# Kernel optimization log

Measured on AMD Instinct MI355X. Metric: run time of the kernel, lower is better.

The kernel has to match this reference:

```python
import jax, jax.numpy as jnp
import numpy as np


def _maxpool2(x):
    # 2x2 max pool, stride 2, on NCHW
    b, c, h, w = x.shape
    return x.reshape(b, c, h // 2, 2, w // 2, 2).max(axis=(3, 5))


def _conv1x1(w, x):
    # w: [out_c, in_c], x: [B, in_c, H, W]
    return jnp.einsum('oc,bchw->bohw', w, x)


def setup_inputs() -> dict:
    key = jax.random.key(0)
    ks = jax.random.split(key, 5)
    B, C, H, W = 16, 64, 64, 64
    x = jax.random.normal(ks[0], (B, C, H, W), dtype=jnp.float32)
    # 1x1 conv weights (spectral-norm treated as already-normalized params)
    Wt = jax.random.normal(ks[1], (C // 8, C), dtype=jnp.float32) * 0.05
    Wp = jax.random.normal(ks[2], (C // 8, C), dtype=jnp.float32) * 0.05
    Wg = jax.random.normal(ks[3], (C // 2, C), dtype=jnp.float32) * 0.05
    Wo = jax.random.normal(ks[4], (C, C // 2), dtype=jnp.float32) * 0.05
    gamma = jnp.float32(0.5)  # nonzero so attention branch contributes
    return {"x": x, "Wt": Wt, "Wp": Wp, "Wg": Wg, "Wo": Wo, "gamma": gamma}


def reference(x, Wt, Wp, Wg, Wo, gamma):
    b, c, h, w = x.shape
    theta = _conv1x1(Wt, x).reshape(b, c // 8, h * w)            # [B, C/8, HW]
    phi = _maxpool2(_conv1x1(Wp, x)).reshape(b, c // 8, -1)      # [B, C/8, HW/4]
    g = _maxpool2(_conv1x1(Wg, x)).reshape(b, c // 2, -1)        # [B, C/2, HW/4]
    # scores: [B, HW, HW/4]; softmax over pooled (key) axis
    beta = jax.nn.softmax(jnp.einsum('bct,bcs->bts', theta, phi), axis=-1)
    o = jnp.einsum('bcs,bts->bct', g, beta).reshape(b, c // 2, h, w)
    o = _conv1x1(Wo, o)                                          # [B, C, H, W]
    return gamma * o + x
```

## Files before the change

kernel.cpp:

```cpp
#include <hip/hip_runtime.h>
#include <math.h>

#define NB   16
#define NC   64
#define HWs  4096
#define NPS  1024
#define LOG2E 1.44269504088896341f

static constexpr size_t PHI_OFF = (size_t)NB * HWs * 8;
static constexpr size_t GT_OFF  = PHI_OFF + (size_t)NB * NPS * 8;
static constexpr size_t Z_OFF   = GT_OFF + (size_t)NB * 32 * NPS;

typedef short s16x8 __attribute__((ext_vector_type(8)));
typedef float f32x4 __attribute__((ext_vector_type(4)));

#define LD8G(p) (*(const s16x8*)(p))

__device__ inline unsigned short f2bf(float f) {
    unsigned int u = __float_as_uint(f);
    u += 0x7fffu + ((u >> 16) & 1u);
    return (unsigned short)(u >> 16);
}
__device__ inline unsigned int pk2(float a, float b) {
    unsigned int ua = __float_as_uint(a); ua += 0x7fffu + ((ua >> 16) & 1u);
    unsigned int ub = __float_as_uint(b); ub += 0x7fffu + ((ub >> 16) & 1u);
    return (ua >> 16) | (ub & 0xffff0000u);
}

__global__ __launch_bounds__(256) void k_proj(
    const float* __restrict__ x, const float* __restrict__ Wt,
    const float* __restrict__ Wp, const float* __restrict__ Wg,
    unsigned short* __restrict__ ws)
{
    __shared__ __align__(16) float xs[64 * 256];
    __shared__ __align__(16) float wlds[48 * 64];

    unsigned short* theta = ws;
    unsigned short* phi   = ws + PHI_OFF;
    unsigned short* gT    = ws + GT_OFF;

    const int tid = threadIdx.x;
    const int blk = blockIdx.x;
    const int b   = blk >> 4;
    const int rg  = blk & 15;

    if (blk == 0 && tid == 0)
        *(uint4*)(ws + Z_OFF) = make_uint4(0u, 0u, 0u, 0u);

    {
        float4* wl4 = (float4*)wlds;
        if (tid < 128) wl4[tid] = ((const float4*)Wt)[tid];
        else           wl4[tid] = ((const float4*)Wp)[tid - 128];
        wl4[256 + tid] = ((const float4*)Wg)[tid];
        wl4[512 + tid] = ((const float4*)Wg)[256 + tid];
    }
    const float* xsrc = x + (size_t)b * NC * HWs + rg * 256;
#pragma unroll
    for (int i = 0; i < 16; ++i) {
        const int f  = i * 256 + tid;
        const int ci = f >> 6;
        const int c4 = f & 63;
        float4 v = *(const float4*)(xsrc + (size_t)ci * HWs + c4 * 4);
        const int e0 = 4 * c4;
        const int r  = e0 >> 6;
        const int c0 = e0 & 63;
        const int qm = r >> 1, dy = r & 1;
        const int q0i = qm * 32 + (c0 >> 1);
        float* base = xs + ci * 256;
        *(float2*)(base + q0i * 4 + dy * 2)       = make_float2(v.x, v.y);
        *(float2*)(base + (q0i + 1) * 4 + dy * 2) = make_float2(v.z, v.w);
    }
    __syncthreads();

    const int outq = __builtin_amdgcn_readfirstlane(tid >> 6);
    const int lane = tid & 63;
    const int qm   = lane >> 5;
    const int qc   = lane & 31;

    f32x4 acc[12];
#pragma unroll
    for (int j = 0; j < 12; ++j)
#pragma unroll
        for (int p = 0; p < 4; ++p) acc[j][p] = 0.f;

    const float* wbase = wlds + outq * 12 * 64;
    for (int cg = 0; cg < 16; ++cg) {
        float4 xv[4];
#pragma unroll
        for (int u = 0; u < 4; ++u)
            xv[u] = *(const float4*)(xs + (cg * 4 + u) * 256 + lane * 4);
#pragma unroll
        for (int j = 0; j < 12; ++j) {
            float4 w4 = *(const float4*)(wbase + j * 64 + cg * 4);
            acc[j][0] += w4.x * xv[0].x + w4.y * xv[1].x + w4.z * xv[2].x + w4.w * xv[3].x;
            acc[j][1] += w4.x * xv[0].y + w4.y * xv[1].y + w4.z * xv[2].y + w4.w * xv[3].y;
            acc[j][2] += w4.x * xv[0].z + w4.y * xv[1].z + w4.z * xv[2].z + w4.w * xv[3].z;
            acc[j][3] += w4.x * xv[0].w + w4.y * xv[1].w + w4.z * xv[2].w + w4.w * xv[3].w;
        }
    }

    const int px00 = (4 * rg + 2 * qm) * 64 + 2 * qc;
    const int ps   = (2 * rg + qm) * 32 + qc;
    const int psP  = (ps & ~63) | (((ps & 15) << 2) | ((ps >> 4) & 3));

    if (outq == 0) {
        const int pxo[4] = {px00, px00 + 1, px00 + 64, px00 + 65};
#pragma unroll
        for (int p = 0; p < 4; ++p) {
            uint4 pkd;
            pkd.x = pk2(acc[0][p] * LOG2E, acc[1][p] * LOG2E);
            pkd.y = pk2(acc[2][p] * LOG2E, acc[3][p] * LOG2E);
            pkd.z = pk2(acc[4][p] * LOG2E, acc[5][p] * LOG2E);
            pkd.w = pk2(acc[6][p] * LOG2E, acc[7][p] * LOG2E);
            *(uint4*)(theta + ((size_t)b * HWs + pxo[p]) * 8) = pkd;
        }
    }
#pragma unroll
    for (int j = 0; j < 12; ++j) {
        const int oo = outq * 12 + j;
        if (oo < 8) continue;
        const float pm = fmaxf(fmaxf(acc[j][0], acc[j][1]), fmaxf(acc[j][2], acc[j][3]));
        if (oo < 16) phi[((size_t)b * NPS + ps) * 8 + (oo - 8)] = f2bf(pm);
        else         gT[((size_t)b * 32 + (oo - 16)) * NPS + psP] = f2bf(pm);
    }
}

__global__ __launch_bounds__(256) void k_attn(
    const float* __restrict__ x, const float* __restrict__ Wo,
    const float* __restrict__ gamma_p, const unsigned short* __restrict__ ws,
    float* __restrict__ out)
{
    __shared__ __align__(16) unsigned char smem[18432];

    const int tid  = threadIdx.x;
    const int wave = __builtin_amdgcn_readfirstlane(tid >> 6);
    const int lane = tid & 63;
    const int quad = lane >> 4, lr = lane & 15;
    const int blk  = blockIdx.x;
    const int b    = blk >> 6;
    const int q0   = (blk & 63) * 64;
    const int qw0  = q0 + wave * 16;

    const unsigned short* th = ws + (size_t)b * HWs * 8;
    const unsigned short* ph = ws + PHI_OFF + (size_t)b * NPS * 8;
    const unsigned short* gp = ws + GT_OFF + (size_t)b * 32 * NPS;
    unsigned short* Pw = (unsigned short*)smem + wave * 2304;

    const s16x8 zf = {0, 0, 0, 0, 0, 0, 0, 0};

    s16x8 thA = zf;
    if (quad == 0) thA = LD8G(th + (size_t)(qw0 + lr) * 8);

    const unsigned short* php;
    int fstep, tstep;
    if (quad == 0) { php = ph + (size_t)lr * 8; fstep = 128; tstep = 512; }
    else           { php = ws + Z_OFF;          fstep = 0;   tstep = 0;   }

    const unsigned short* gb0 = gp + (size_t)lr * NPS + quad * 8;
    const unsigned short* gb1 = gb0 + (size_t)16 * NPS;

    f32x4 O[2];
    f32x4 l4;
#pragma unroll
    for (int r = 0; r < 4; ++r) { O[0][r] = 0.f; O[1][r] = 0.f; l4[r] = 0.f; }

    s16x8 Gc[4], Gn[4];
    const f32x4 zc = {0.f, 0.f, 0.f, 0.f};

#pragma unroll
    for (int t = 0; t < 16; ++t) {
        s16x8 phB[4];
        phB[0] = LD8G(php);
        phB[1] = LD8G(php + fstep);
        phB[2] = LD8G(php + 2 * fstep);
        phB[3] = LD8G(php + 3 * fstep);
        php += tstep;

        Gn[0] = LD8G(gb0);
        Gn[1] = LD8G(gb1);
        Gn[2] = LD8G(gb0 + 32);
        Gn[3] = LD8G(gb1 + 32);
        gb0 += 64; gb1 += 64;

        if (t > 0) {
            const unsigned short* Pb = Pw + ((t - 1) & 1) * 1152 + lr * 72 + quad * 8;
            s16x8 Pf0 = *(const s16x8*)(Pb);
            s16x8 Pf1 = *(const s16x8*)(Pb + 32);
            O[0] = __builtin_amdgcn_mfma_f32_16x16x32_bf16(Pf0, Gc[0], O[0], 0, 0, 0);
            O[1] = __builtin_amdgcn_mfma_f32_16x16x32_bf16(Pf0, Gc[1], O[1], 0, 0, 0);
            O[0] = __builtin_amdgcn_mfma_f32_16x16x32_bf16(Pf1, Gc[2], O[0], 0, 0, 0);
            O[1] = __builtin_amdgcn_mfma_f32_16x16x32_bf16(Pf1, Gc[3], O[1], 0, 0, 0);
        }

        f32x4 S[4];
#pragma unroll
        for (int ss = 0; ss < 4; ++ss)
            S[ss] = __builtin_amdgcn_mfma_f32_16x16x32_bf16(thA, phB[ss], zc, 0, 0, 0);

        unsigned short* Pbw = Pw + (t & 1) * 1152;
#pragma unroll
        for (int r = 0; r < 4; ++r) {
            const float p0 = __builtin_amdgcn_exp2f(S[0][r]);
            const float p1 = __builtin_amdgcn_exp2f(S[1][r]);
            const float p2 = __builtin_amdgcn_exp2f(S[2][r]);
            const float p3 = __builtin_amdgcn_exp2f(S[3][r]);
            l4[r] += (p0 + p1) + (p2 + p3);
            uint2 pw;
            pw.x = (__float_as_uint(p0) >> 16) | (__float_as_uint(p1) & 0xffff0000u);
            pw.y = (__float_as_uint(p2) >> 16) | (__float_as_uint(p3) & 0xffff0000u);
            *(uint2*)(Pbw + (quad * 4 + r) * 72 + lr * 4) = pw;
        }

        Gc[0] = Gn[0]; Gc[1] = Gn[1]; Gc[2] = Gn[2]; Gc[3] = Gn[3];
    }
    {
        const unsigned short* Pb = Pw + 1152 + lr * 72 + quad * 8;
        s16x8 Pf0 = *(const s16x8*)(Pb);
        s16x8 Pf1 = *(const s16x8*)(Pb + 32);
        O[0] = __builtin_amdgcn_mfma_f32_16x16x32_bf16(Pf0, Gc[0], O[0], 0, 0, 0);
        O[1] = __builtin_amdgcn_mfma_f32_16x16x32_bf16(Pf0, Gc[1], O[1], 0, 0, 0);
        O[0] = __builtin_amdgcn_mfma_f32_16x16x32_bf16(Pf1, Gc[2], O[0], 0, 0, 0);
        O[1] = __builtin_amdgcn_mfma_f32_16x16x32_bf16(Pf1, Gc[3], O[1], 0, 0, 0);
    }

    f32x4 linv;
#pragma unroll
    for (int r = 0; r < 4; ++r) {
        float v = l4[r];
        v += __shfl_xor(v, 1);
        v += __shfl_xor(v, 2);
        v += __shfl_xor(v, 4);
        v += __shfl_xor(v, 8);
        linv[r] = 1.f / v;
    }

    __syncthreads();
    float* otile = (float*)smem;
#pragma unroll
    for (int cs = 0; cs < 2; ++cs) {
        f32x4 v;
#pragma unroll
        for (int r = 0; r < 4; ++r) v[r] = O[cs][r] * linv[r];
        *(f32x4*)(otile + (cs * 16 + lr) * 68 + wave * 16 + quad * 4) = v;
    }
    __syncthreads();

    const int qq = tid & 63;
    const int quarter = __builtin_amdgcn_readfirstlane(tid >> 6);
    float acc[16];
#pragma unroll
    for (int j = 0; j < 16; ++j) acc[j] = 0.f;
    for (int c = 0; c < 32; ++c) {
        const float ov = otile[c * 68 + qq];
#pragma unroll
        for (int j = 0; j < 16; ++j)
            acc[j] += Wo[(quarter * 16 + j) * 32 + c] * ov;
    }
    const float gam = gamma_p[0];
#pragma unroll
    for (int j = 0; j < 16; ++j) {
        const size_t a = ((size_t)b * NC + quarter * 16 + j) * HWs + q0 + qq;
        out[a] = gam * acc[j] + x[a];
    }
}

extern "C" void kernel_launch(void* const* d_in, const int* in_sizes, int n_in,
                              void* d_out, int out_size, void* d_ws, size_t ws_size,
                              hipStream_t stream) {
    const float* x     = (const float*)d_in[0];
    const float* Wt    = (const float*)d_in[1];
    const float* Wp    = (const float*)d_in[2];
    const float* Wg    = (const float*)d_in[3];
    const float* Wo    = (const float*)d_in[4];
    const float* gamma = (const float*)d_in[5];
    float* out = (float*)d_out;
    unsigned short* ws = (unsigned short*)d_ws;

    k_proj<<<256, 256, 0, stream>>>(x, Wt, Wp, Wg, ws);
    k_attn<<<1024, 256, 0, stream>>>(x, Wo, gamma, ws, out);
}
```

Measured before the change: 134.3 us.

## Stage phi and g tiles cooperatively through double-buffered LDS in attention kernel

In the attention kernel, each wave used to read phi and gT straight from global memory. Now the block loads them cooperatively into double-buffered shared memory, using register prefetch of the next tile and a block barrier each iteration. The goal is to stop the four waves from each re-reading the same keys and values from global or L2. In exchange it adds shared memory, which can lower occupancy, and 16 __syncthreads per block.

Result: no change. 134.2 us (-0.1%).

```diff
diff --git a/kernel.cpp b/kernel.cpp
--- a/kernel.cpp
+++ b/kernel.cpp
@@ -130,7 +130,7 @@
     const float* __restrict__ gamma_p, const unsigned short* __restrict__ ws,
     float* __restrict__ out)
 {
-    __shared__ __align__(16) unsigned char smem[18432];
+    __shared__ __align__(16) unsigned char smem[29952];
 
     const int tid  = threadIdx.x;
     const int wave = __builtin_amdgcn_readfirstlane(tid >> 6);
@@ -144,20 +144,35 @@
     const unsigned short* th = ws + (size_t)b * HWs * 8;
     const unsigned short* ph = ws + PHI_OFF + (size_t)b * NPS * 8;
     const unsigned short* gp = ws + GT_OFF + (size_t)b * 32 * NPS;
+
     unsigned short* Pw = (unsigned short*)smem + wave * 2304;
 
+    const int sc   = tid >> 3;
+    const int sseg = tid & 7;
+    const unsigned short* gsrc = gp + (size_t)sc * NPS + sseg * 8;
+    const unsigned short* psrc = ph + (size_t)tid * 8;
+    unsigned char* gdstB = smem + 20480 + sc * 144 + sseg * 16;
+    unsigned char* pdstB = smem + 18432 + tid * 16;
+
+    if (tid < 4) ((unsigned int*)(smem + 29696))[tid] = 0u;
+
+    {
+        uint4 gv = *(const uint4*)(gsrc);
+        *(uint4*)(gdstB) = gv;
+        if (tid < 64) {
+            uint4 pv = *(const uint4*)(psrc);
+            *(uint4*)(pdstB) = pv;
+        }
+    }
+
     const s16x8 zf = {0, 0, 0, 0, 0, 0, 0, 0};
-
     s16x8 thA = zf;
     if (quad == 0) thA = LD8G(th + (size_t)(qw0 + lr) * 8);
 
-    const unsigned short* php;
-    int fstep, tstep;
-    if (quad == 0) { php = ph + (size_t)lr * 8; fstep = 128; tstep = 512; }
-    else           { php = ws + Z_OFF;          fstep = 0;   tstep = 0;   }
-
-    const unsigned short* gb0 = gp + (size_t)lr * NPS + quad * 8;
-    const unsigned short* gb1 = gb0 + (size_t)16 * NPS;
+    const int phb_base    = (quad == 0) ? (18432 + lr * 16) : 29696;
+    const int phb_bufstep = (quad == 0) ? 1024 : 0;
+    const int phb_ssstep  = (quad == 0) ? 256  : 0;
+    const int g_base      = 20480 + lr * 144 + quad * 16;
 
     f32x4 O[2];
     f32x4 l4;
@@ -167,20 +182,29 @@
     s16x8 Gc[4], Gn[4];
     const f32x4 zc = {0.f, 0.f, 0.f, 0.f};
 
+    __syncthreads();
+
 #pragma unroll
     for (int t = 0; t < 16; ++t) {
-        s16x8 phB[4];
-        phB[0] = LD8G(php);
-        phB[1] = LD8G(php + fstep);
-        phB[2] = LD8G(php + 2 * fstep);
-        phB[3] = LD8G(php + 3 * fstep);
-        php += tstep;
-
-        Gn[0] = LD8G(gb0);
-        Gn[1] = LD8G(gb1);
-        Gn[2] = LD8G(gb0 + 32);
-        Gn[3] = LD8G(gb1 + 32);
-        gb0 += 64; gb1 += 64;
+        const int buf  = t & 1;
+        const int nbuf = buf ^ 1;
+
+        uint4 gv = {0,0,0,0}, pv = {0,0,0,0};
+        if (t < 15) {
+            gv = *(const uint4*)(gsrc + (t + 1) * 64);
+            if (tid < 64) pv = *(const uint4*)(psrc + (t + 1) * 512);
+        }
+
+        const unsigned char* pb = smem + phb_base + buf * phb_bufstep;
+        s16x8 phB0 = *(const s16x8*)(pb);
+        s16x8 phB1 = *(const s16x8*)(pb + phb_ssstep);
+        s16x8 phB2 = *(const s16x8*)(pb + 2 * phb_ssstep);
+        s16x8 phB3 = *(const s16x8*)(pb + 3 * phb_ssstep);
+        const unsigned char* gb = smem + g_base + buf * 4608;
+        Gn[0] = *(const s16x8*)(gb);
+        Gn[1] = *(const s16x8*)(gb + 2304);
+        Gn[2] = *(const s16x8*)(gb + 64);
+        Gn[3] = *(const s16x8*)(gb + 2304+64);
 
         if (t > 0) {
             const unsigned short* Pb = Pw + ((t - 1) & 1) * 1152 + lr * 72 + quad * 8;
@@ -193,11 +217,12 @@
         }
 
         f32x4 S[4];
-#pragma unroll
-        for (int ss = 0; ss < 4; ++ss)
-            S[ss] = __builtin_amdgcn_mfma_f32_16x16x32_bf16(thA, phB[ss], zc, 0, 0, 0);
-
-        unsigned short* Pbw = Pw + (t & 1) * 1152;
+        S[0] = __builtin_amdgcn_mfma_f32_16x16x32_bf16(thA, phB0, zc, 0, 0, 0);
+        S[1] = __builtin_amdgcn_mfma_f32_16x16x32_bf16(thA, phB1, zc, 0, 0, 0);
+        S[2] = __builtin_amdgcn_mfma_f32_16x16x32_bf16(thA, phB2, zc, 0, 0, 0);
+        S[3] = __builtin_amdgcn_mfma_f32_16x16x32_bf16(thA, phB3, zc, 0, 0, 0);
+
+        unsigned short* Pbw = Pw + buf * 1152;
 #pragma unroll
         for (int r = 0; r < 4; ++r) {
             const float p0 = __builtin_amdgcn_exp2f(S[0][r]);
@@ -211,7 +236,14 @@
             *(uint2*)(Pbw + (quad * 4 + r) * 72 + lr * 4) = pw;
         }
 
+        if (t < 15) {
+            *(uint4*)(gdstB + nbuf * 4608) = gv;
+            if (tid < 64) *(uint4*)(pdstB + nbuf * 1024) = pv;
+        }
+
         Gc[0] = Gn[0]; Gc[1] = Gn[1]; Gc[2] = Gn[2]; Gc[3] = Gn[3];
+
+        __syncthreads();
     }
     {
         const unsigned short* Pb = Pw + 1152 + lr * 72 + quad * 8;
```
